# Kernel tuning notes

Hardware: AMD Instinct MI355X
Metric: run time of the kernel (lower is better)

The kernel has to match this reference:

```python
import jax, jax.numpy as jnp
import numpy as np

NEG_INF = -9e15
ALPHA = 0.2  # leaky_relu slope


def gat_layer(h, adj, e_feat, W, We, a_s, a_d, a_e, h_res):
    """Dense multi-head GAT layer with edge features.
    h: [B,N,Fin], adj: [B,N,N] (0/1), e_feat: [B,N,N,Ein]
    W: [H,Fin,Fout], We: [H,Ein,Eout], a_s/a_d: [H,Fout], a_e: [H,Eout]
    Returns head-averaged (x_prime [B,N,Fout], e_prime [B,N,N,Eout]).
    """
    Wh = jnp.einsum('bnf,hfo->bhno', h, W)            # [B,H,N,Fout]
    Me = jnp.einsum('bnmf,hfe->bhnme', e_feat, We)    # [B,H,N,N,Eout]
    s_src = jnp.einsum('bhno,ho->bhn', Wh, a_s)
    s_dst = jnp.einsum('bhno,ho->bhn', Wh, a_d)
    s_edge = jnp.einsum('bhnme,he->bhnm', Me, a_e)
    scores = jax.nn.leaky_relu(s_src[:, :, :, None] + s_dst[:, :, None, :] + s_edge, ALPHA)
    scores = jnp.where(adj[:, None, :, :] > 0, scores, NEG_INF)
    att = jax.nn.softmax(scores, axis=-1)             # [B,H,N,N]
    h_prime = jnp.einsum('bhnm,bhmo->bhno', att, Wh)
    h_prime = jax.nn.elu(h_prime) + h_res[:, None]    # concat=True -> elu; residual add
    e_prime = att[..., None] * Me                      # attention-modulated edge features
    return h_prime.mean(axis=1), e_prime.mean(axis=1)


def setup_inputs() -> dict:
    key = jax.random.key(0)
    ks = jax.random.split(key, 16)
    B, N, F, E, H = 2, 256, 768, 7, 2
    nhid, ehid = 768, 768 // 2
    sc = lambda fan: 1.0 / np.sqrt(fan)
    return {
        'x': jax.random.normal(ks[0], (B, N, F), jnp.float32),
        'adj': jax.random.randint(ks[1], (B, N, N), 0, 2, jnp.int32),
        'e': jax.random.uniform(ks[2], (B, N, N, E), jnp.float32),
        'W1': jax.random.normal(ks[3], (H, F, nhid), jnp.float32) * sc(F),
        'We1': jax.random.normal(ks[4], (H, E, ehid), jnp.float32) * sc(E),
        'a1s': jax.random.normal(ks[5], (H, nhid), jnp.float32) * sc(nhid),
        'a1d': jax.random.normal(ks[6], (H, nhid), jnp.float32) * sc(nhid),
        'a1e': jax.random.normal(ks[7], (H, ehid), jnp.float32) * sc(ehid),
        'W2': jax.random.normal(ks[8], (H, nhid, nhid), jnp.float32) * sc(nhid),
        'We2': jax.random.normal(ks[9], (H, ehid, ehid), jnp.float32) * sc(ehid),
        'a2s': jax.random.normal(ks[10], (H, nhid), jnp.float32) * sc(nhid),
        'a2d': jax.random.normal(ks[11], (H, nhid), jnp.float32) * sc(nhid),
        'a2e': jax.random.normal(ks[12], (H, ehid), jnp.float32) * sc(ehid),
    }


def reference(x, adj, e, W1, We1, a1s, a1d, a1e, W2, We2, a2s, a2d, a2e):
    # dropout layers are identity in eval mode
    x1, e1 = gat_layer(x, adj, e, W1, We1, a1s, a1d, a1e, x)
    x2, e2 = gat_layer(x1, adj, e1, W2, We2, a2s, a2d, a2e, x)
    return x2, e2
```

## Files before the change

kernel.cpp:

```cpp
#include <hip/hip_runtime.h>
#include <hip/hip_bf16.h>
#include <cstddef>


typedef __attribute__((ext_vector_type(8))) short bf16x8;
typedef __attribute__((ext_vector_type(4))) short bf16x4;
typedef __attribute__((ext_vector_type(4))) float f32x4;
typedef unsigned short us;

#define DEVINL static __device__ __forceinline__

DEVINL us f2bf(float f) {
    union { float f; unsigned u; } v; v.f = f;
    return (us)((v.u + 0x7FFFu + ((v.u >> 16) & 1u)) >> 16);
}
DEVINL float bf2f(us b) {
    union { unsigned u; float f; } v; v.u = ((unsigned)b) << 16; return v.f;
}
DEVINL float wredmax(float v) {
#pragma unroll
    for (int s = 32; s; s >>= 1) v = fmaxf(v, __shfl_xor(v, s));
    return v;
}
DEVINL float wredsum(float v) {
#pragma unroll
    for (int s = 32; s; s >>= 1) v += __shfl_xor(v, s);
    return v;
}

DEVINL void transpose_body(const float* __restrict__ W, us* __restrict__ WT, int bb) {
    __shared__ us tile[64][65];
    const int ft = (bb % 12) * 64, ot = ((bb / 12) % 12) * 64, h = bb / 144;
    const int t = threadIdx.x;
    const float* Wh = W + (size_t)h * 589824;
    us* WTh = WT + (size_t)h * 589824;
#pragma unroll
    for (int i = 0; i < 16; i++) {
        int idx = t + i * 256, r = idx >> 6, c = idx & 63;
        tile[c][r] = f2bf(Wh[(size_t)(ft + r) * 768 + ot + c]);
    }
    __syncthreads();
#pragma unroll
    for (int i = 0; i < 2; i++) {
        int idx = t + i * 256, r = idx >> 3, c0 = (idx & 7) * 8;
        us pk[8];
#pragma unroll
        for (int j = 0; j < 8; j++) pk[j] = tile[r][c0 + j];
        *(bf16x8*)&WTh[(size_t)(ot + r) * 768 + ft + c0] = *(bf16x8*)pk;
    }
}

DEVINL void mcat_body(const float* __restrict__ We1, const float* __restrict__ We2,
                      float* __restrict__ Mcat, int h2, int tct) {
    __shared__ float we1L[16][384];
    __shared__ float part[16][128];
    const int t = threadIdx.x;
    for (int i = t; i < 6144; i += 256) {
        int m = i / 384, o = i % 384;
        int h1 = m >> 3, kk = m & 7;
        we1L[m][o] = (kk < 7) ? We1[(h1 * 7 + kk) * 384 + o] : 0.0f;
    }
    __syncthreads();
    const int tc = tct * 128 + (t & 127);
    const int half = t >> 7;
    float acc[16];
#pragma unroll
    for (int m = 0; m < 16; m++) acc[m] = 0.0f;
    const float* w2 = We2 + (size_t)h2 * 147456 + tc;
    for (int o = half * 192; o < half * 192 + 192; o++) {
        float wv = w2[(size_t)o * 384];
#pragma unroll
        for (int m = 0; m < 16; m++) acc[m] += we1L[m][o] * wv;
    }
    if (half == 1)
#pragma unroll
        for (int m = 0; m < 16; m++) part[m][t & 127] = acc[m];
    __syncthreads();
    if (half == 0) {
#pragma unroll
        for (int m = 0; m < 16; m++) {
            float v = 0.25f * (acc[m] + part[m][t]);
            int h1 = m >> 3, kk = m & 7;
            Mcat[((h1 * 2 + h2) * 8 + kk) * 384 + tc] = v;
        }
    }
}

DEVINL void pre_qu_body(const float* __restrict__ W1, const float* __restrict__ W2,
                        const float* __restrict__ We1,
                        const float* __restrict__ a1s, const float* __restrict__ a1d,
                        const float* __restrict__ a1e, const float* __restrict__ a2s,
                        const float* __restrict__ a2d,
                        float* __restrict__ q, float* __restrict__ u1, int blk) {
    const int g = blk * 32 + (threadIdx.x >> 3);
    const int lane = threadIdx.x & 7;
    float acc = 0.0f;
    if (g < 6144) {
        int vec = g / 1536, rem = g % 1536, h = rem / 768, f = rem % 768;
        const float* W = (vec < 2) ? W1 : W2;
        const float* a = (vec == 0) ? a1s : (vec == 1) ? a1d : (vec == 2) ? a2s : a2d;
        const float* wr = W + (size_t)(h * 768 + f) * 768;
        const float* ar = a + h * 768;
        for (int o = lane; o < 768; o += 8) acc += wr[o] * ar[o];
        for (int s = 4; s; s >>= 1) acc += __shfl_down(acc, s, 8);
        if (lane == 0) q[g] = acc;
    } else if (g < 6160) {
        int g2 = g - 6144, h = g2 >> 3, k = g2 & 7;
        if (k < 7) {
            const float* wr = We1 + (h * 7 + k) * 384;
            const float* ar = a1e + h * 384;
            for (int o = lane; o < 384; o += 8) acc += wr[o] * ar[o];
        }
        for (int s = 4; s; s >>= 1) acc += __shfl_down(acc, s, 8);
        if (lane == 0) u1[g2] = acc;
    }
}

DEVINL void cvt_body(const float* __restrict__ in, us* __restrict__ out, int blk) {
    int i = (blk * 256 + threadIdx.x) * 8;
    float4 v0 = *(const float4*)&in[i];
    float4 v1 = *(const float4*)&in[i + 4];
    us pk[8] = {f2bf(v0.x), f2bf(v0.y), f2bf(v0.z), f2bf(v0.w),
                f2bf(v1.x), f2bf(v1.y), f2bf(v1.z), f2bf(v1.w)};
    *(bf16x8*)&out[i] = *(bf16x8*)pk;
}

DEVINL void wcalc_body(const float* __restrict__ Mcat, const float* __restrict__ a2e,
                       float* __restrict__ w) {
    const int t = threadIdx.x, g = t >> 3, lane = t & 7;
    int hh = g >> 3, k = g & 7, h2 = hh & 1;
    float acc = 0.0f;
    if (k < 7)
        for (int o = lane; o < 384; o += 8) acc += Mcat[(hh * 8 + k) * 384 + o] * a2e[h2 * 384 + o];
    for (int s = 4; s; s >>= 1) acc += __shfl_down(acc, s, 8);
    if (lane == 0) w[g] = 2.0f * acc;
}

DEVINL void bfrag_body(const float* __restrict__ Mcat, us* __restrict__ Bfrag, int ct) {
    const int l = threadIdx.x;
    if (l < 64) {
        us pk[8];
#pragma unroll
        for (int j = 0; j < 8; j++)
            pk[j] = f2bf(Mcat[((l >> 4) * 8 + j) * 384 + ct * 16 + (l & 15)]);
        *(bf16x8*)&Bfrag[(ct * 64 + l) * 8] = *(bf16x8*)pk;
    }
}

DEVINL void sdots_body(const float* __restrict__ x, const float* __restrict__ qs,
                       const float* __restrict__ qd, float* __restrict__ out_s,
                       float* __restrict__ out_d, int n, int b) {
    const int t = threadIdx.x, wv = t >> 6;
    const float* xr = x + (size_t)(b * 256 + n) * 768;
    float a0 = 0, a1 = 0, a2 = 0, a3 = 0;
#pragma unroll
    for (int i = 0; i < 3; i++) {
        int k = i * 256 + t;
        float xv = xr[k];
        a0 += xv * qs[k];
        a1 += xv * qs[768 + k];
        a2 += xv * qd[k];
        a3 += xv * qd[768 + k];
    }
    a0 = wredsum(a0); a1 = wredsum(a1); a2 = wredsum(a2); a3 = wredsum(a3);
    __shared__ float part[4][4];
    if ((t & 63) == 0) { part[wv][0] = a0; part[wv][1] = a1; part[wv][2] = a2; part[wv][3] = a3; }
    __syncthreads();
    if (t == 0) {
        float r0 = 0, r1 = 0, r2 = 0, r3 = 0;
#pragma unroll
        for (int i = 0; i < 4; i++) { r0 += part[i][0]; r1 += part[i][1]; r2 += part[i][2]; r3 += part[i][3]; }
        out_s[(b * 2 + 0) * 256 + n] = r0;
        out_s[(b * 2 + 1) * 256 + n] = r1;
        out_d[(b * 2 + 0) * 256 + n] = r2;
        out_d[(b * 2 + 1) * 256 + n] = r3;
    }
}

DEVINL void att1_body(const float* __restrict__ e, const int* __restrict__ adj,
                      const float* __restrict__ s_s, const float* __restrict__ s_d,
                      const float* __restrict__ u1, us* __restrict__ attb,
                      int n, int bb) {
    __shared__ float eL[1792];
    __shared__ float smax[2][4], ssum[2][4];
    const int t = threadIdx.x, wv = t >> 6;
    const float* erow = e + (size_t)(bb * 256 + n) * 1792;
#pragma unroll
    for (int i = 0; i < 7; i++) eL[t + i * 256] = erow[t + i * 256];
    __syncthreads();
    float ss0 = s_s[(bb * 2 + 0) * 256 + n], ss1 = s_s[(bb * 2 + 1) * 256 + n];
    float sd0 = s_d[(bb * 2 + 0) * 256 + t], sd1 = s_d[(bb * 2 + 1) * 256 + t];
    float se0 = 0, se1 = 0;
#pragma unroll
    for (int k = 0; k < 7; k++) {
        float ev = eL[t * 7 + k];
        se0 += ev * u1[k];
        se1 += ev * u1[8 + k];
    }
    float sc0 = ss0 + sd0 + se0, sc1 = ss1 + sd1 + se1;
    sc0 = sc0 > 0.0f ? sc0 : 0.2f * sc0;
    sc1 = sc1 > 0.0f ? sc1 : 0.2f * sc1;
    bool ok = adj[(size_t)(bb * 256 + n) * 256 + t] > 0;
    sc0 = ok ? sc0 : -9e15f;
    sc1 = ok ? sc1 : -9e15f;
    float w0 = wredmax(sc0), w1 = wredmax(sc1);
    if ((t & 63) == 0) { smax[0][wv] = w0; smax[1][wv] = w1; }
    __syncthreads();
    float mx0 = fmaxf(fmaxf(smax[0][0], smax[0][1]), fmaxf(smax[0][2], smax[0][3]));
    float mx1 = fmaxf(fmaxf(smax[1][0], smax[1][1]), fmaxf(smax[1][2], smax[1][3]));
    float ex0 = __expf(sc0 - mx0), ex1 = __expf(sc1 - mx1);
    float su0 = wredsum(ex0), su1 = wredsum(ex1);
    if ((t & 63) == 0) { ssum[0][wv] = su0; ssum[1][wv] = su1; }
    __syncthreads();
    float i0 = 1.0f / (ssum[0][0] + ssum[0][1] + ssum[0][2] + ssum[0][3]);
    float i1 = 1.0f / (ssum[1][0] + ssum[1][1] + ssum[1][2] + ssum[1][3]);
    attb[((size_t)(bb * 2 + 0) * 256 + n) * 256 + t] = f2bf(ex0 * i0);
    attb[((size_t)(bb * 2 + 1) * 256 + n) * 256 + t] = f2bf(ex1 * i1);
}

DEVINL void att2_body(const float* __restrict__ e, const int* __restrict__ adj,
                      const float* __restrict__ s_s, const float* __restrict__ s_d,
                      const float* __restrict__ w, const us* __restrict__ att1b,
                      us* __restrict__ attb, int n, int bb) {
    __shared__ float eL[1792];
    __shared__ float smax[2][4], ssum[2][4];
    const int t = threadIdx.x, wv = t >> 6;
    const float* erow = e + (size_t)(bb * 256 + n) * 1792;
#pragma unroll
    for (int i = 0; i < 7; i++) eL[t + i * 256] = erow[t + i * 256];
    __syncthreads();
    float ss0 = s_s[(bb * 2 + 0) * 256 + n], ss1 = s_s[(bb * 2 + 1) * 256 + n];
    float sd0 = s_d[(bb * 2 + 0) * 256 + t], sd1 = s_d[(bb * 2 + 1) * 256 + t];
    float a10 = bf2f(att1b[((size_t)(bb * 2 + 0) * 256 + n) * 256 + t]);
    float a11 = bf2f(att1b[((size_t)(bb * 2 + 1) * 256 + n) * 256 + t]);
    float ew00 = 0, ew01 = 0, ew10 = 0, ew11 = 0;
#pragma unroll
    for (int k = 0; k < 7; k++) {
        float ev = eL[t * 7 + k];
        ew00 += ev * w[k];
        ew01 += ev * w[8 + k];
        ew10 += ev * w[16 + k];
        ew11 += ev * w[24 + k];
    }
    float sc0 = ss0 + sd0 + a10 * ew00 + a11 * ew10;
    float sc1 = ss1 + sd1 + a10 * ew01 + a11 * ew11;
    sc0 = sc0 > 0.0f ? sc0 : 0.2f * sc0;
    sc1 = sc1 > 0.0f ? sc1 : 0.2f * sc1;
    bool ok = adj[(size_t)(bb * 256 + n) * 256 + t] > 0;
    sc0 = ok ? sc0 : -9e15f;
    sc1 = ok ? sc1 : -9e15f;
    float w0 = wredmax(sc0), w1 = wredmax(sc1);
    if ((t & 63) == 0) { smax[0][wv] = w0; smax[1][wv] = w1; }
    __syncthreads();
    float mx0 = fmaxf(fmaxf(smax[0][0], smax[0][1]), fmaxf(smax[0][2], smax[0][3]));
    float mx1 = fmaxf(fmaxf(smax[1][0], smax[1][1]), fmaxf(smax[1][2], smax[1][3]));
    float ex0 = __expf(sc0 - mx0), ex1 = __expf(sc1 - mx1);
    float su0 = wredsum(ex0), su1 = wredsum(ex1);
    if ((t & 63) == 0) { ssum[0][wv] = su0; ssum[1][wv] = su1; }
    __syncthreads();
    float i0 = 1.0f / (ssum[0][0] + ssum[0][1] + ssum[0][2] + ssum[0][3]);
    float i1 = 1.0f / (ssum[1][0] + ssum[1][1] + ssum[1][2] + ssum[1][3]);
    attb[((size_t)(bb * 2 + 0) * 256 + n) * 256 + t] = f2bf(ex0 * i0);
    attb[((size_t)(bb * 2 + 1) * 256 + n) * 256 + t] = f2bf(ex1 * i1);
}

DEVINL void gemm_xw_body(const us* __restrict__ A, const us* __restrict__ BT,
                         us* __restrict__ WhT, int mt, int ot, int h) {
    const int t = threadIdx.x, wv = t >> 6, l = t & 63;
    const int wm = wv >> 1, wn = wv & 1, lr = l & 15, lk = l >> 4;
    __shared__ us As[64][40];
    __shared__ us Bs[64][40];
    const int arow = t >> 2, acol = (t & 3) * 8;
    const us* Bh = BT + (size_t)h * 589824;
    f32x4 acc[2][2];
#pragma unroll
    for (int i = 0; i < 2; i++)
#pragma unroll
        for (int j = 0; j < 2; j++) acc[i][j] = (f32x4){0, 0, 0, 0};
    for (int k0 = 0; k0 < 768; k0 += 32) {
        __syncthreads();
        *(bf16x8*)&As[arow][acol] = *(const bf16x8*)&A[(size_t)(mt * 64 + arow) * 768 + k0 + acol];
        *(bf16x8*)&Bs[arow][acol] = *(const bf16x8*)&Bh[(size_t)(ot * 64 + arow) * 768 + k0 + acol];
        __syncthreads();
        bf16x8 af[2], bfv[2];
#pragma unroll
        for (int i = 0; i < 2; i++) af[i] = *(const bf16x8*)&As[wm * 32 + i * 16 + lr][lk * 8];
#pragma unroll
        for (int j = 0; j < 2; j++) bfv[j] = *(const bf16x8*)&Bs[wn * 32 + j * 16 + lr][lk * 8];
#pragma unroll
        for (int i = 0; i < 2; i++)
#pragma unroll
            for (int j = 0; j < 2; j++)
                acc[i][j] = __builtin_amdgcn_mfma_f32_16x16x32_bf16(af[i], bfv[j], acc[i][j], 0, 0, 0);
    }
#pragma unroll
    for (int i = 0; i < 2; i++)
#pragma unroll
        for (int j = 0; j < 2; j++) {
            int n0 = mt * 64 + wm * 32 + i * 16 + lk * 4;
            int og = ot * 64 + wn * 32 + j * 16 + lr;
            int b = n0 >> 8, n = n0 & 255;
            us pk[4];
#pragma unroll
            for (int r = 0; r < 4; r++) pk[r] = f2bf(acc[i][j][r]);
            *(bf16x4*)&WhT[((size_t)(b * 2 + h) * 768 + og) * 256 + n] = *(bf16x4*)pk;
        }
}

DEVINL void gemm_att_body(const us* __restrict__ attb, const us* __restrict__ WhT,
                          const float* __restrict__ resid, float* __restrict__ xout,
                          us* __restrict__ xbout, int mt, int ot, int b) {
    const int t = threadIdx.x, wv = t >> 6, l = t & 63;
    const int wm = wv >> 1, wn = wv & 1, lr = l & 15, lk = l >> 4;
    __shared__ us As2[32][40];
    __shared__ us Bs2[64][40];
    float res[2][4] = {};
    for (int h = 0; h < 2; h++) {
        const us* Ah = attb + (size_t)(b * 2 + h) * 65536;
        const us* Bh = WhT + (size_t)(b * 2 + h) * 196608;
        f32x4 acc[2];
        acc[0] = (f32x4){0, 0, 0, 0};
        acc[1] = (f32x4){0, 0, 0, 0};
        for (int k0 = 0; k0 < 256; k0 += 32) {
            __syncthreads();
            if (t < 128) {
                int ar = t >> 2, ac = (t & 3) * 8;
                *(bf16x8*)&As2[ar][ac] = *(const bf16x8*)&Ah[(size_t)(mt * 32 + ar) * 256 + k0 + ac];
            }
            {
                int br = t >> 2, bc = (t & 3) * 8;
                *(bf16x8*)&Bs2[br][bc] = *(const bf16x8*)&Bh[(size_t)(ot * 64 + br) * 256 + k0 + bc];
            }
            __syncthreads();
            bf16x8 af = *(const bf16x8*)&As2[wm * 16 + lr][lk * 8];
#pragma unroll
            for (int j = 0; j < 2; j++) {
                bf16x8 bv = *(const bf16x8*)&Bs2[wn * 32 + j * 16 + lr][lk * 8];
                acc[j] = __builtin_amdgcn_mfma_f32_16x16x32_bf16(af, bv, acc[j], 0, 0, 0);
            }
        }
#pragma unroll
        for (int j = 0; j < 2; j++)
#pragma unroll
            for (int r = 0; r < 4; r++) {
                float v = acc[j][r];
                res[j][r] += (v > 0.0f ? v : (expf(v) - 1.0f));
            }
        __syncthreads();
    }
#pragma unroll
    for (int j = 0; j < 2; j++) {
        int n0 = mt * 32 + wm * 16 + lk * 4;
        int og = ot * 64 + wn * 32 + j * 16 + lr;
#pragma unroll
        for (int r = 0; r < 4; r++) {
            size_t idx = (size_t)(b * 256 + n0 + r) * 768 + og;
            float v = 0.5f * res[j][r] + resid[idx];
            if (xout) xout[idx] = v;
            if (xbout) xbout[idx] = f2bf(v);
        }
    }
}

DEVINL void e2row_body(const float* __restrict__ e, const us* __restrict__ att1b,
                       const us* __restrict__ att2b, const us* __restrict__ Bfrag,
                       float* __restrict__ e2out, int bb, int n) {
    __shared__ us blB[1536 * 8];
    __shared__ float eL[1792];
    __shared__ float aL[4][256];
    const int t = threadIdx.x;
    for (int i = t; i < 1536; i += 256)
        *(bf16x8*)&blB[i * 8] = *(const bf16x8*)&Bfrag[(size_t)i * 8];
    const float* erow = e + (size_t)(bb * 256 + n) * 1792;
#pragma unroll
    for (int i = 0; i < 7; i++) eL[t + i * 256] = erow[t + i * 256];
    const size_t abase = (size_t)bb * 131072 + n * 256;
    aL[0][t] = bf2f(att1b[abase + t]);
    aL[1][t] = bf2f(att1b[abase + 65536 + t]);
    aL[2][t] = bf2f(att2b[abase + t]);
    aL[3][t] = bf2f(att2b[abase + 65536 + t]);
    __syncthreads();
    const int wv = t >> 6, l = t & 63, le = l & 15, lq = l >> 4;
    const int h1 = lq >> 1, h2 = lq & 1;
    bf16x8 av[4];
#pragma unroll
    for (int g = 0; g < 4; g++) {
        int m = g * 64 + wv * 16 + le;
        float c = aL[h1][m] * aL[2 + h2][m];
        us pk[8];
#pragma unroll
        for (int j = 0; j < 7; j++) pk[j] = f2bf(c * eL[m * 7 + j]);
        pk[7] = 0;
        av[g] = *(bf16x8*)pk;
    }
    const f32x4 zero = {0, 0, 0, 0};
    const size_t rowbase = (size_t)bb * 65536 + n * 256;
#pragma unroll
    for (int cg = 0; cg < 3; cg++) {
        bf16x8 bfr[8];
#pragma unroll
        for (int i = 0; i < 8; i++) bfr[i] = *(const bf16x8*)&blB[(cg * 512 + i * 64 + l) * 8];
        for (int g = 0; g < 4; g++) {
            size_t eidx = rowbase + g * 64 + wv * 16 + le;
#pragma unroll
            for (int i = 0; i < 8; i++) {
                f32x4 acc = __builtin_amdgcn_mfma_f32_16x16x32_bf16(bfr[i], av[g], zero, 0, 0, 0);
                *(f32x4*)&e2out[eidx * 384 + cg * 128 + i * 16 + lq * 4] = acc;
            }
        }
    }
}

__global__ __launch_bounds__(256) void stage1(
    const float* W1, const float* W2, const float* We1, const float* We2,
    const float* a1s, const float* a1d, const float* a1e,
    const float* a2s, const float* a2d, const float* x,
    us* W1T, us* W2T, us* xb, float* q, float* u1, float* Mcat) {
    int b = blockIdx.x;
    if (b < 6)          mcat_body(We1, We2, Mcat, b & 1, b >> 1);
    else if (b < 199)   pre_qu_body(W1, W2, We1, a1s, a1d, a1e, a2s, a2d, q, u1, b - 6);
    else if (b < 487)   transpose_body(W1, W1T, b - 199);
    else if (b < 775)   transpose_body(W2, W2T, b - 487);
    else                cvt_body(x, xb, b - 775);
}

__global__ __launch_bounds__(256) void stage2(
    const float* Mcat, const float* a2e, float* wbuf, us* Bfrag,
    const float* x, const float* qs, const float* qd, float* s1s, float* s1d) {
    int b = blockIdx.x;
    if (b < 1)        wcalc_body(Mcat, a2e, wbuf);
    else if (b < 25)  bfrag_body(Mcat, Bfrag, b - 1);
    else { int i = b - 25; sdots_body(x, qs, qd, s1s, s1d, i & 255, i >> 8); }
}

__global__ __launch_bounds__(256) void stage3(
    const float* e, const int* adj, const float* s1s, const float* s1d,
    const float* u1, us* att1b, const us* xb, const us* W1T, us* WhT1) {
    int b = blockIdx.x;
    if (b < 512) att1_body(e, adj, s1s, s1d, u1, att1b, b & 255, b >> 8);
    else { int g = b - 512; gemm_xw_body(xb, W1T, WhT1, g & 7, (g >> 3) % 12, g / 96); }
}

__global__ __launch_bounds__(256) void stage4(
    const us* att1b, const us* WhT1, const float* x, float* x1, us* xb1) {
    int b = blockIdx.x;
    gemm_att_body(att1b, WhT1, x, x1, xb1, b & 7, (b >> 3) % 12, b / 96);
}

__global__ __launch_bounds__(256) void stage5(
    const float* x1, const float* qs, const float* qd, float* s2s, float* s2d,
    const us* xb1, const us* W2T, us* WhT2) {
    int b = blockIdx.x;
    if (b < 512) sdots_body(x1, qs, qd, s2s, s2d, b & 255, b >> 8);
    else { int g = b - 512; gemm_xw_body(xb1, W2T, WhT2, g & 7, (g >> 3) % 12, g / 96); }
}

__global__ __launch_bounds__(256) void stage6(
    const float* e, const int* adj, const float* s2s, const float* s2d,
    const float* wbuf, const us* att1b, us* att2b) {
    int b = blockIdx.x;
    att2_body(e, adj, s2s, s2d, wbuf, att1b, att2b, b & 255, b >> 8);
}

__global__ __launch_bounds__(256) void stage7(
    const us* att2b, const us* WhT2, const float* x, float* x2out,
    const float* e, const us* att1b, const us* Bfrag, float* e2out) {
    int b = blockIdx.x;
    if (b < 192) gemm_att_body(att2b, WhT2, x, x2out, (us*)nullptr, b & 7, (b >> 3) % 12, b / 96);
    else { int r = b - 192; e2row_body(e, att1b, att2b, Bfrag, e2out, r >> 8, r & 255); }
}

extern "C" void kernel_launch(void* const* d_in, const int* in_sizes, int n_in,
                              void* d_out, int out_size, void* d_ws, size_t ws_size,
                              hipStream_t stream) {
    const float* x   = (const float*)d_in[0];
    const int*   adj = (const int*)d_in[1];
    const float* e   = (const float*)d_in[2];
    const float* W1  = (const float*)d_in[3];
    const float* We1 = (const float*)d_in[4];
    const float* a1s = (const float*)d_in[5];
    const float* a1d = (const float*)d_in[6];
    const float* a1e = (const float*)d_in[7];
    const float* W2  = (const float*)d_in[8];
    const float* We2 = (const float*)d_in[9];
    const float* a2s = (const float*)d_in[10];
    const float* a2d = (const float*)d_in[11];
    const float* a2e = (const float*)d_in[12];

    float* out   = (float*)d_out;
    float* x2out = out;
    float* e2out = out + 393216;

    char* ws = (char*)d_ws;
    float* q     = (float*)(ws + 0);
    float* u1    = (float*)(ws + 24576);
    float* wbuf  = (float*)(ws + 24640);
    float* Mcat  = (float*)(ws + 24832);
    us*    Bfrag = (us*)(ws + 73984);
    float* s1s   = (float*)(ws + 98560);
    float* s1d   = (float*)(ws + 102656);
    float* s2s   = (float*)(ws + 106752);
    float* s2d   = (float*)(ws + 110848);
    us*    att1b = (us*)(ws + 114944);
    us*    att2b = (us*)(ws + 639232);
    us*    W1T   = (us*)(ws + 1163520);
    us*    W2T   = (us*)(ws + 3522816);
    us*    xb    = (us*)(ws + 5882112);
    us*    xb1   = (us*)(ws + 6668544);
    us*    WhT1  = (us*)(ws + 7454976);
    us*    WhT2  = (us*)(ws + 9027840);
    float* x1    = (float*)(ws + 10600704);

    stage1<<<967, 256, 0, stream>>>(W1, W2, We1, We2, a1s, a1d, a1e, a2s, a2d,
                                    x, W1T, W2T, xb, q, u1, Mcat);
    stage2<<<537, 256, 0, stream>>>(Mcat, a2e, wbuf, Bfrag, x, q + 0, q + 1536, s1s, s1d);
    stage3<<<704, 256, 0, stream>>>(e, adj, s1s, s1d, u1, att1b, xb, W1T, WhT1);
    stage4<<<192, 256, 0, stream>>>(att1b, WhT1, x, x1, xb1);
    stage5<<<704, 256, 0, stream>>>(x1, q + 3072, q + 4608, s2s, s2d, xb1, W2T, WhT2);
    stage6<<<512, 256, 0, stream>>>(e, adj, s2s, s2d, wbuf, att1b, att2b);
    stage7<<<704, 256, 0, stream>>>(att2b, WhT2, x, x2out, e, att1b, Bfrag, e2out);
}
```

Baseline: 114.1 us.

## Fuse layer-2 attention softmax into e2 and att@Wh kernels, drop stage7

Removes the separate layer-2 attention kernel and its att2b round-trip. The e2 row blocks now compute the layer-2 softmax in place. A new set of 16 wide blocks recomputes the softmax for 32-row tiles and then runs the full att@Wh GEMM across all 12 output tiles and both heads. This saves one kernel launch and a global write and read of the attention matrix. The cost is redundant softmax computation and only 16 blocks doing the whole x2 GEMM serially, which may become the critical path.

```diff
diff --git a/kernel.cpp b/kernel.cpp
--- a/kernel.cpp
+++ b/kernel.cpp
@@ -218,52 +218,6 @@
     attb[((size_t)(bb * 2 + 1) * 256 + n) * 256 + t] = f2bf(ex1 * i1);
 }
 
-DEVINL void att2_body(const float* __restrict__ e, const int* __restrict__ adj,
-                      const float* __restrict__ s_s, const float* __restrict__ s_d,
-                      const float* __restrict__ w, const us* __restrict__ att1b,
-                      us* __restrict__ attb, int n, int bb) {
-    __shared__ float eL[1792];
-    __shared__ float smax[2][4], ssum[2][4];
-    const int t = threadIdx.x, wv = t >> 6;
-    const float* erow = e + (size_t)(bb * 256 + n) * 1792;
-#pragma unroll
-    for (int i = 0; i < 7; i++) eL[t + i * 256] = erow[t + i * 256];
-    __syncthreads();
-    float ss0 = s_s[(bb * 2 + 0) * 256 + n], ss1 = s_s[(bb * 2 + 1) * 256 + n];
-    float sd0 = s_d[(bb * 2 + 0) * 256 + t], sd1 = s_d[(bb * 2 + 1) * 256 + t];
-    float a10 = bf2f(att1b[((size_t)(bb * 2 + 0) * 256 + n) * 256 + t]);
-    float a11 = bf2f(att1b[((size_t)(bb * 2 + 1) * 256 + n) * 256 + t]);
-    float ew00 = 0, ew01 = 0, ew10 = 0, ew11 = 0;
-#pragma unroll
-    for (int k = 0; k < 7; k++) {
-        float ev = eL[t * 7 + k];
-        ew00 += ev * w[k];
-        ew01 += ev * w[8 + k];
-        ew10 += ev * w[16 + k];
-        ew11 += ev * w[24 + k];
-    }
-    float sc0 = ss0 + sd0 + a10 * ew00 + a11 * ew10;
-    float sc1 = ss1 + sd1 + a10 * ew01 + a11 * ew11;
-    sc0 = sc0 > 0.0f ? sc0 : 0.2f * sc0;
-    sc1 = sc1 > 0.0f ? sc1 : 0.2f * sc1;
-    bool ok = adj[(size_t)(bb * 256 + n) * 256 + t] > 0;
-    sc0 = ok ? sc0 : -9e15f;
-    sc1 = ok ? sc1 : -9e15f;
-    float w0 = wredmax(sc0), w1 = wredmax(sc1);
-    if ((t & 63) == 0) { smax[0][wv] = w0; smax[1][wv] = w1; }
-    __syncthreads();
-    float mx0 = fmaxf(fmaxf(smax[0][0], smax[0][1]), fmaxf(smax[0][2], smax[0][3]));
-    float mx1 = fmaxf(fmaxf(smax[1][0], smax[1][1]), fmaxf(smax[1][2], smax[1][3]));
-    float ex0 = __expf(sc0 - mx0), ex1 = __expf(sc1 - mx1);
-    float su0 = wredsum(ex0), su1 = wredsum(ex1);
-    if ((t & 63) == 0) { ssum[0][wv] = su0; ssum[1][wv] = su1; }
-    __syncthreads();
-    float i0 = 1.0f / (ssum[0][0] + ssum[0][1] + ssum[0][2] + ssum[0][3]);
-    float i1 = 1.0f / (ssum[1][0] + ssum[1][1] + ssum[1][2] + ssum[1][3]);
-    attb[((size_t)(bb * 2 + 0) * 256 + n) * 256 + t] = f2bf(ex0 * i0);
-    attb[((size_t)(bb * 2 + 1) * 256 + n) * 256 + t] = f2bf(ex1 * i1);
-}
-
 DEVINL void gemm_xw_body(const us* __restrict__ A, const us* __restrict__ BT,
                          us* __restrict__ WhT, int mt, int ot, int h) {
     const int t = threadIdx.x, wv = t >> 6, l = t & 63;
@@ -362,23 +316,58 @@
     }
 }
 
-DEVINL void e2row_body(const float* __restrict__ e, const us* __restrict__ att1b,
-                       const us* __restrict__ att2b, const us* __restrict__ Bfrag,
-                       float* __restrict__ e2out, int bb, int n) {
+DEVINL void att2e2_body(const float* __restrict__ e, const int* __restrict__ adj,
+                        const float* __restrict__ s_s, const float* __restrict__ s_d,
+                        const float* __restrict__ w, const us* __restrict__ att1b,
+                        const us* __restrict__ Bfrag, float* __restrict__ e2out,
+                        int bb, int n) {
     __shared__ us blB[1536 * 8];
     __shared__ float eL[1792];
-    __shared__ float aL[4][256];
-    const int t = threadIdx.x;
+    __shared__ float aL1[2][256], aL2[2][256];
+    __shared__ float smax[2][4], ssum[2][4];
+    const int t = threadIdx.x, wv4 = t >> 6;
     for (int i = t; i < 1536; i += 256)
         *(bf16x8*)&blB[i * 8] = *(const bf16x8*)&Bfrag[(size_t)i * 8];
     const float* erow = e + (size_t)(bb * 256 + n) * 1792;
 #pragma unroll
     for (int i = 0; i < 7; i++) eL[t + i * 256] = erow[t + i * 256];
-    const size_t abase = (size_t)bb * 131072 + n * 256;
-    aL[0][t] = bf2f(att1b[abase + t]);
-    aL[1][t] = bf2f(att1b[abase + 65536 + t]);
-    aL[2][t] = bf2f(att2b[abase + t]);
-    aL[3][t] = bf2f(att2b[abase + 65536 + t]);
+    const size_t a1base = (size_t)bb * 131072 + n * 256;
+    float a10 = bf2f(att1b[a1base + t]);
+    float a11 = bf2f(att1b[a1base + 65536 + t]);
+    aL1[0][t] = a10;
+    aL1[1][t] = a11;
+    __syncthreads();
+    float ss0 = s_s[(bb * 2 + 0) * 256 + n], ss1 = s_s[(bb * 2 + 1) * 256 + n];
+    float sd0 = s_d[(bb * 2 + 0) * 256 + t], sd1 = s_d[(bb * 2 + 1) * 256 + t];
+    float ew00 = 0, ew01 = 0, ew10 = 0, ew11 = 0;
+#pragma unroll
+    for (int k = 0; k < 7; k++) {
+        float ev = eL[t * 7 + k];
+        ew00 += ev * w[k];
+        ew01 += ev * w[8 + k];
+        ew10 += ev * w[16 + k];
+        ew11 += ev * w[24 + k];
+    }
+    float sc0 = ss0 + sd0 + a10 * ew00 + a11 * ew10;
+    float sc1 = ss1 + sd1 + a10 * ew01 + a11 * ew11;
+    sc0 = sc0 > 0.0f ? sc0 : 0.2f * sc0;
+    sc1 = sc1 > 0.0f ? sc1 : 0.2f * sc1;
+    bool ok = adj[(size_t)(bb * 256 + n) * 256 + t] > 0;
+    sc0 = ok ? sc0 : -9e15f;
+    sc1 = ok ? sc1 : -9e15f;
+    float w0 = wredmax(sc0), w1 = wredmax(sc1);
+    if ((t & 63) == 0) { smax[0][wv4] = w0; smax[1][wv4] = w1; }
+    __syncthreads();
+    float mx0 = fmaxf(fmaxf(smax[0][0], smax[0][1]), fmaxf(smax[0][2], smax[0][3]));
+    float mx1 = fmaxf(fmaxf(smax[1][0], smax[1][1]), fmaxf(smax[1][2], smax[1][3]));
+    float ex0 = __expf(sc0 - mx0), ex1 = __expf(sc1 - mx1);
+    float su0 = wredsum(ex0), su1 = wredsum(ex1);
+    if ((t & 63) == 0) { ssum[0][wv4] = su0; ssum[1][wv4] = su1; }
+    __syncthreads();
+    float i0 = 1.0f / (ssum[0][0] + ssum[0][1] + ssum[0][2] + ssum[0][3]);
+    float i1 = 1.0f / (ssum[1][0] + ssum[1][1] + ssum[1][2] + ssum[1][3]);
+    aL2[0][t] = ex0 * i0;
+    aL2[1][t] = ex1 * i1;
     __syncthreads();
     const int wv = t >> 6, l = t & 63, le = l & 15, lq = l >> 4;
     const int h1 = lq >> 1, h2 = lq & 1;
@@ -386,7 +375,7 @@
 #pragma unroll
     for (int g = 0; g < 4; g++) {
         int m = g * 64 + wv * 16 + le;
-        float c = aL[h1][m] * aL[2 + h2][m];
+        float c = aL1[h1][m] * aL2[h2][m];
         us pk[8];
 #pragma unroll
         for (int j = 0; j < 7; j++) pk[j] = f2bf(c * eL[m * 7 + j]);
@@ -406,6 +395,103 @@
             for (int i = 0; i < 8; i++) {
                 f32x4 acc = __builtin_amdgcn_mfma_f32_16x16x32_bf16(bfr[i], av[g], zero, 0, 0, 0);
                 *(f32x4*)&e2out[eidx * 384 + cg * 128 + i * 16 + lq * 4] = acc;
+            }
+        }
+    }
+}
+
+DEVINL void gemm_att2_fat(const float* __restrict__ e, const int* __restrict__ adj,
+                          const float* __restrict__ s2s, const float* __restrict__ s2d,
+                          const float* __restrict__ wbuf, const us* __restrict__ att1b,
+                          const us* __restrict__ WhT2, const float* __restrict__ resid,
+                          float* __restrict__ x2out, int mt, int b) {
+    __shared__ us aA[2][32][264];
+    const int t = threadIdx.x, wv = t >> 6, l = t & 63;
+    for (int rr = 0; rr < 8; rr++) {
+        const int r = wv * 8 + rr, n = mt * 32 + r, m0 = l * 4;
+        const float* ep = e + ((size_t)(b * 256 + n) * 256 + m0) * 7;
+        float ev[4][7];
+#pragma unroll
+        for (int mm = 0; mm < 4; mm++)
+#pragma unroll
+            for (int k = 0; k < 7; k++) ev[mm][k] = ep[mm * 7 + k];
+        const int* adjp = adj + (size_t)(b * 256 + n) * 256 + m0;
+        float ss0 = s2s[(b * 2 + 0) * 256 + n], ss1 = s2s[(b * 2 + 1) * 256 + n];
+        float sc0[4], sc1[4];
+#pragma unroll
+        for (int mm = 0; mm < 4; mm++) {
+            int m = m0 + mm;
+            float sd0 = s2d[(b * 2 + 0) * 256 + m];
+            float sd1 = s2d[(b * 2 + 1) * 256 + m];
+            float a10 = bf2f(att1b[((size_t)(b * 2 + 0) * 256 + n) * 256 + m]);
+            float a11 = bf2f(att1b[((size_t)(b * 2 + 1) * 256 + n) * 256 + m]);
+            float ew00 = 0, ew01 = 0, ew10 = 0, ew11 = 0;
+#pragma unroll
+            for (int k = 0; k < 7; k++) {
+                float evk = ev[mm][k];
+                ew00 += evk * wbuf[k];
+                ew01 += evk * wbuf[8 + k];
+                ew10 += evk * wbuf[16 + k];
+                ew11 += evk * wbuf[24 + k];
+            }
+            float s0 = ss0 + sd0 + a10 * ew00 + a11 * ew10;
+            float s1 = ss1 + sd1 + a10 * ew01 + a11 * ew11;
+            s0 = s0 > 0.0f ? s0 : 0.2f * s0;
+            s1 = s1 > 0.0f ? s1 : 0.2f * s1;
+            bool ok = adjp[mm] > 0;
+            sc0[mm] = ok ? s0 : -9e15f;
+            sc1[mm] = ok ? s1 : -9e15f;
+        }
+        float mx0 = fmaxf(fmaxf(sc0[0], sc0[1]), fmaxf(sc0[2], sc0[3]));
+        float mx1 = fmaxf(fmaxf(sc1[0], sc1[1]), fmaxf(sc1[2], sc1[3]));
+        mx0 = wredmax(mx0); mx1 = wredmax(mx1);
+        float ex0[4], ex1[4], su0 = 0, su1 = 0;
+#pragma unroll
+        for (int mm = 0; mm < 4; mm++) {
+            ex0[mm] = __expf(sc0[mm] - mx0); su0 += ex0[mm];
+            ex1[mm] = __expf(sc1[mm] - mx1); su1 += ex1[mm];
+        }
+        su0 = wredsum(su0); su1 = wredsum(su1);
+        float i0 = 1.0f / su0, i1 = 1.0f / su1;
+        us p0[4], p1[4];
+#pragma unroll
+        for (int mm = 0; mm < 4; mm++) { p0[mm] = f2bf(ex0[mm] * i0); p1[mm] = f2bf(ex1[mm] * i1); }
+        *(bf16x4*)&aA[0][r][m0] = *(bf16x4*)p0;
+        *(bf16x4*)&aA[1][r][m0] = *(bf16x4*)p1;
+    }
+    __syncthreads();
+    const int wm = wv >> 1, wn = wv & 1, lr = l & 15, lk = l >> 4;
+    for (int ot = 0; ot < 12; ot++) {
+        float res[2][4] = {};
+        for (int h = 0; h < 2; h++) {
+            const us* Bh = WhT2 + (size_t)(b * 2 + h) * 196608;
+            f32x4 acc[2];
+            acc[0] = (f32x4){0, 0, 0, 0};
+            acc[1] = (f32x4){0, 0, 0, 0};
+            for (int k0 = 0; k0 < 256; k0 += 32) {
+                bf16x8 af = *(const bf16x8*)&aA[h][wm * 16 + lr][k0 + lk * 8];
+#pragma unroll
+                for (int j = 0; j < 2; j++) {
+                    bf16x8 bv = *(const bf16x8*)&Bh[(size_t)(ot * 64 + wn * 32 + j * 16 + lr) * 256 + k0 + lk * 8];
+                    acc[j] = __builtin_amdgcn_mfma_f32_16x16x32_bf16(af, bv, acc[j], 0, 0, 0);
+                }
+            }
+#pragma unroll
+            for (int j = 0; j < 2; j++)
+#pragma unroll
+                for (int r = 0; r < 4; r++) {
+                    float v = acc[j][r];
+                    res[j][r] += (v > 0.0f ? v : (expf(v) - 1.0f));
+                }
+        }
+#pragma unroll
+        for (int j = 0; j < 2; j++) {
+            int n0 = mt * 32 + wm * 16 + lk * 4;
+            int og = ot * 64 + wn * 32 + j * 16 + lr;
+#pragma unroll
+            for (int r = 0; r < 4; r++) {
+                size_t idx = (size_t)(b * 256 + n0 + r) * 768 + og;
+                x2out[idx] = 0.5f * res[j][r] + resid[idx];
             }
         }
     }
@@ -457,17 +543,13 @@
 
 __global__ __launch_bounds__(256) void stage6(
     const float* e, const int* adj, const float* s2s, const float* s2d,
-    const float* wbuf, const us* att1b, us* att2b) {
+    const float* wbuf, const us* att1b, const us* Bfrag, float* e2out,
+    const us* WhT2, const float* x, float* x2out) {
     int b = blockIdx.x;
-    att2_body(e, adj, s2s, s2d, wbuf, att1b, att2b, b & 255, b >> 8);
-}
-
-__global__ __launch_bounds__(256) void stage7(
-    const us* att2b, const us* WhT2, const float* x, float* x2out,
-    const float* e, const us* att1b, const us* Bfrag, float* e2out) {
-    int b = blockIdx.x;
-    if (b < 192) gemm_att_body(att2b, WhT2, x, x2out, (us*)nullptr, b & 7, (b >> 3) % 12, b / 96);
-    else { int r = b - 192; e2row_body(e, att1b, att2b, Bfrag, e2out, r >> 8, r & 255); }
+    if (b < 16) gemm_att2_fat(e, adj, s2s, s2d, wbuf, att1b, WhT2, x, x2out,
+                              b >> 1, b & 1);
+    else { int r = b - 16; att2e2_body(e, adj, s2s, s2d, wbuf, att1b, Bfrag, e2out,
+                                       r >> 8, r & 255); }
 }
 
 extern "C" void kernel_launch(void* const* d_in, const int* in_sizes, int n_in,
@@ -502,7 +584,6 @@
     float* s2s   = (float*)(ws + 106752);
     float* s2d   = (float*)(ws + 110848);
     us*    att1b = (us*)(ws + 114944);
-    us*    att2b = (us*)(ws + 639232);
     us*    W1T   = (us*)(ws + 1163520);
     us*    W2T   = (us*)(ws + 3522816);
     us*    xb    = (us*)(ws + 5882112);
@@ -517,6 +598,6 @@
     stage3<<<704, 256, 0, stream>>>(e, adj, s1s, s1d, u1, att1b, xb, W1T, WhT1);
     stage4<<<192, 256, 0, stream>>>(att1b, WhT1, x, x1, xb1);
     stage5<<<704, 256, 0, stream>>>(x1, q + 3072, q + 4608, s2s, s2d, xb1, W2T, WhT2);
-    stage6<<<512, 256, 0, stream>>>(e, adj, s2s, s2d, wbuf, att1b, att2b);
-    stage7<<<704, 256, 0, stream>>>(att2b, WhT2, x, x2out, e, att1b, Bfrag, e2out);
-}
+    stage6<<<528, 256, 0, stream>>>(e, adj, s2s, s2d, wbuf, att1b, Bfrag, e2out,
+                                    WhT2, x, x2out);
+}
```

After: 152.6 us. 1.34x slower.
